# Performance work log

Measured on AMD Instinct MI355X. Metric: run time of the kernel, lower is better.

## Reference

```python
import jax, jax.numpy as jnp
import numpy as np

B, S, D = 4, 2048, 1024
H = 16
HD = D // H  # 64
MASKED_BIAS = jnp.float32(-10000.0)


def setup_inputs() -> dict:
    key = jax.random.key(0)
    ks = jax.random.split(key, 5)
    std = 0.02
    return {
        "hidden_states": jax.random.normal(ks[0], (B, S, D), jnp.float32),
        "Wq": jax.random.normal(ks[1], (D, D), jnp.float32) * std,
        "bq": jnp.zeros((D,), jnp.float32),
        "Wk": jax.random.normal(ks[2], (D, D), jnp.float32) * std,
        "bk": jnp.zeros((D,), jnp.float32),
        "Wv": jax.random.normal(ks[3], (D, D), jnp.float32) * std,
        "bv": jnp.zeros((D,), jnp.float32),
        "Wo": jax.random.normal(ks[4], (D, D), jnp.float32) * std,
        "bo": jnp.zeros((D,), jnp.float32),
    }


def _split_heads(x):
    # [B, S, D] -> [B, H, S, HD]
    return x.reshape(B, S, H, HD).transpose(0, 2, 1, 3)


def reference(hidden_states, Wq, bq, Wk, bk, Wv, bv, Wo, bo):
    q = _split_heads(hidden_states @ Wq + bq)
    k = _split_heads(hidden_states @ Wk + bk)
    v = _split_heads(hidden_states @ Wv + bv)

    # scores [B, H, S, S], scaled by sqrt(head_dim) (scale=True)
    w = jnp.einsum("bhqd,bhkd->bhqk", q, k) / jnp.sqrt(jnp.float32(HD))
    causal = jnp.tril(jnp.ones((S, S), dtype=bool))  # [S, S]
    w = jnp.where(causal[None, None], w, MASKED_BIAS)
    w = jax.nn.softmax(w, axis=-1)
    # attn_pdrop = 0.0 -> dropout is identity

    a = jnp.einsum("bhqk,bhkd->bhqd", w, v)  # [B, H, S, HD]
    a = a.transpose(0, 2, 1, 3).reshape(B, S, D)  # merge heads
    out = a @ Wo + bo
    # resid_pdrop = 0.0 -> identity
    return out
```

## Files before the change

kernel.cpp:

```cpp
#include <hip/hip_runtime.h>
#include <stdint.h>

typedef unsigned short u16;
typedef __bf16 bf16x2 __attribute__((ext_vector_type(2)));
typedef __bf16 bf16x8 __attribute__((ext_vector_type(8)));
typedef float f32x4 __attribute__((ext_vector_type(4)));
typedef float f32x16 __attribute__((ext_vector_type(16)));
typedef unsigned int u32x4 __attribute__((ext_vector_type(4)));
typedef u16 u16x8 __attribute__((ext_vector_type(8)));
typedef u16 u16x4 __attribute__((ext_vector_type(4)));

#define MFMA16(a, b, c) __builtin_amdgcn_mfma_f32_16x16x32_bf16((a), (b), (c), 0, 0, 0)
#define MFMA32(a, b, c) __builtin_amdgcn_mfma_f32_32x32x16_bf16((a), (b), (c), 0, 0, 0)

#define QSCALE 0.18033688011112042f

#if defined(__has_builtin)
#if __has_builtin(__builtin_amdgcn_exp2f)
#define EXP2(x) __builtin_amdgcn_exp2f(x)
#endif
#endif
#ifndef EXP2
#define EXP2(x) __expf((x) * 0.6931471805599453f)
#endif

__device__ __forceinline__ u16 f2bf(float f) {
  return __builtin_bit_cast(u16, (__bf16)f);
}

__device__ __forceinline__ unsigned cvtpk(float lo, float hi) {
  bf16x2 t;
  t[0] = (__bf16)lo;
  t[1] = (__bf16)hi;
  return __builtin_bit_cast(unsigned, t);
}

__device__ __forceinline__ bf16x8 load_frag(const u16* lds_base, int byteoff) {
  u32x4 v = *(const u32x4*)((const char*)lds_base + byteoff);
  return __builtin_bit_cast(bf16x8, v);
}

#define GLOAD_LDS16(gp, lp)                                                        \
  __builtin_amdgcn_global_load_lds((const __attribute__((address_space(1))) void*)(gp), \
                                   (__attribute__((address_space(3))) void*)(lp), 16, 0, 0)

template <int ROWS>
__device__ __forceinline__ void stage_tile(const u16* __restrict__ src, int ld, u16* lds,
                                           int tid) {
  constexpr int SLOTS = ROWS * 8;
#pragma unroll
  for (int it = 0; it < SLOTS / 256; ++it) {
    const int s = it * 256 + tid;
    const int row = s >> 3;
    const int seg = (s & 7) ^ (row & 7);
    const u16* g = src + row * ld + seg * 8;
    u16* l = lds + (it * 256 + (tid & ~63)) * 8;
    GLOAD_LDS16(g, l);
  }
}


__global__ __launch_bounds__(256) void cvt_x(const float* __restrict__ in,
                                             u16* __restrict__ out) {
  const int i = (int)blockIdx.x * 256 + (int)threadIdx.x;
  const float4 a = ((const float4*)in)[2 * i];
  const float4 b = ((const float4*)in)[2 * i + 1];
  u16x8 o;
  o[0] = f2bf(a.x); o[1] = f2bf(a.y); o[2] = f2bf(a.z); o[3] = f2bf(a.w);
  o[4] = f2bf(b.x); o[5] = f2bf(b.y); o[6] = f2bf(b.z); o[7] = f2bf(b.w);
  ((u16x8*)out)[i] = o;
}

__global__ __launch_bounds__(256) void cvt_w_t(const float* __restrict__ W,
                                               u16* __restrict__ Wt) {
  __shared__ u16 t[64][65];
  const int tid = (int)threadIdx.x;
  const int r = tid >> 2;
  const int cs = (tid & 3) * 16;
  const int tr = (int)blockIdx.y * 64;
  const int tc = (int)blockIdx.x * 64;
#pragma unroll
  for (int i = 0; i < 16; i += 4) {
    const float4 v = *(const float4*)&W[(size_t)(tr + r) * 1024 + tc + cs + i];
    t[r][cs + i + 0] = f2bf(v.x);
    t[r][cs + i + 1] = f2bf(v.y);
    t[r][cs + i + 2] = f2bf(v.z);
    t[r][cs + i + 3] = f2bf(v.w);
  }
  __syncthreads();
  u16 tmp[16];
#pragma unroll
  for (int i = 0; i < 16; ++i) tmp[i] = t[cs + i][r];
  u16x8 o0, o1;
#pragma unroll
  for (int i = 0; i < 8; ++i) { o0[i] = tmp[i]; o1[i] = tmp[8 + i]; }
  *(u16x8*)&Wt[(size_t)(tc + r) * 1024 + tr + cs] = o0;
  *(u16x8*)&Wt[(size_t)(tc + r) * 1024 + tr + cs + 8] = o1;
}


__device__ __forceinline__ size_t vfrag_addr(int row, int col) {
  const int b = row >> 11, s = row & 2047;
  const int h = col >> 6, d = col & 63;
  return ((size_t)((b * 16 + h) * 32 + (s >> 6))) * 4096 + (size_t)(d >> 5) * 2048 +
         (size_t)((s & 63) >> 4) * 512 + (size_t)((d & 31) | (((s >> 3) & 1) << 5)) * 8 +
         (s & 7);
}

__device__ __forceinline__ size_t kfrag_addr(int row, int col) {
  const int b = row >> 11, s = row & 2047;
  const int h = col >> 6, d = col & 63;
  return ((size_t)((b * 16 + h) * 64 + (s >> 5))) * 2048 + (size_t)(d >> 4) * 512 +
         (size_t)((s & 31) | (((d >> 3) & 1) << 5)) * 8 + (d & 7);
}


__device__ __forceinline__ void gemm_core(const u16* __restrict__ Abase,
                                          const u16* __restrict__ Bbase, u16* lds, int tid,
                                          int wm, int wn, int lr, int lg,
                                          f32x4 (&acc)[4][4]) {
  constexpr int K = 1024;
  for (int k0 = 0; k0 < K; k0 += 64) {
    stage_tile<128>(Abase + k0, K, lds, tid);
    stage_tile<128>(Bbase + k0, K, lds + 128 * 64, tid);
    __syncthreads();
#pragma unroll
    for (int ks = 0; ks < 2; ++ks) {
      bf16x8 af[4], bf[4];
#pragma unroll
      for (int i = 0; i < 4; ++i) {
        const int ar = wm * 64 + i * 16 + lr;
        af[i] = load_frag(lds, ar * 128 + ((ks * 64 + lg * 16) ^ ((ar & 7) << 4)));
        const int br = wn * 64 + i * 16 + lr;
        bf[i] = load_frag(lds + 128 * 64, br * 128 + ((ks * 64 + lg * 16) ^ ((br & 7) << 4)));
      }
#pragma unroll
      for (int mf = 0; mf < 4; ++mf)
#pragma unroll
        for (int nf = 0; nf < 4; ++nf) acc[mf][nf] = MFMA16(af[mf], bf[nf], acc[mf][nf]);
    }
    __syncthreads();
  }
}


__global__ __launch_bounds__(256) void gemm_qkv(const u16* __restrict__ A,
                                                const u16* __restrict__ Bq,
                                                const u16* __restrict__ Bk,
                                                const u16* __restrict__ Bv,
                                                const float* __restrict__ bq,
                                                const float* __restrict__ bk,
                                                const float* __restrict__ bv,
                                                u16* __restrict__ Qo, u16* __restrict__ Ko,
                                                u16* __restrict__ Vo) {
  __shared__ __align__(16) u16 lds[2 * 128 * 64];
  const int tid = (int)threadIdx.x;
  const int w = tid >> 6, lane = tid & 63;
  const int wm = w >> 1, wn = w & 1;
  const int lr = lane & 15, lg = lane >> 4;
  const int g = (int)blockIdx.x;
  const int m_idx = g >> 3, nt = g & 7;
  const int mt = (int)blockIdx.y;

  const u16* Bt = m_idx == 0 ? Bq : (m_idx == 1 ? Bk : Bv);
  const float* bias = m_idx == 0 ? bq : (m_idx == 1 ? bk : bv);

  f32x4 acc[4][4] = {};
  gemm_core(A + (size_t)mt * 128 * 1024, Bt + (size_t)nt * 128 * 1024, lds, tid, wm, wn, lr,
            lg, acc);

#pragma unroll
  for (int mf = 0; mf < 4; ++mf) {
#pragma unroll
    for (int nf = 0; nf < 4; ++nf) {
      const int col = nt * 128 + wn * 64 + nf * 16 + lr;
      const float bv2 = bias[col];
#pragma unroll
      for (int r = 0; r < 4; ++r) {
        const int row = mt * 128 + wm * 64 + mf * 16 + lg * 4 + r;
        const float v = acc[mf][nf][r] + bv2;
        if (m_idx == 0) {
          Qo[(size_t)row * 1024 + col] = f2bf(v * QSCALE);
        } else if (m_idx == 1) {
          Ko[kfrag_addr(row, col)] = f2bf(v);
        } else {
          Vo[vfrag_addr(row, col)] = f2bf(v);
        }
      }
    }
  }
}


__global__ __launch_bounds__(256) void gemm_out(const u16* __restrict__ A,
                                                const u16* __restrict__ Bt,
                                                const float* __restrict__ bias,
                                                float* __restrict__ Cout) {
  __shared__ __align__(16) u16 lds[2 * 128 * 64];
  const int tid = (int)threadIdx.x;
  const int w = tid >> 6, lane = tid & 63;
  const int wm = w >> 1, wn = w & 1;
  const int lr = lane & 15, lg = lane >> 4;
  const int mt = (int)blockIdx.y, nt = (int)blockIdx.x;

  f32x4 acc[4][4] = {};
  gemm_core(A + (size_t)mt * 128 * 1024, Bt + (size_t)nt * 128 * 1024, lds, tid, wm, wn, lr,
            lg, acc);

#pragma unroll
  for (int mf = 0; mf < 4; ++mf) {
#pragma unroll
    for (int nf = 0; nf < 4; ++nf) {
      const int col = nt * 128 + wn * 64 + nf * 16 + lr;
      const float bv = bias[col];
#pragma unroll
      for (int r = 0; r < 4; ++r) {
        const int row = mt * 128 + wm * 64 + mf * 16 + lg * 4 + r;
        Cout[(size_t)row * 1024 + col] = acc[mf][nf][r] + bv;
      }
    }
  }
}


__device__ __forceinline__ void loadK(bf16x8 (&kf)[2][4], const u16* __restrict__ p) {
#pragma unroll
  for (int sb = 0; sb < 2; ++sb)
#pragma unroll
    for (int dk = 0; dk < 4; ++dk)
      kf[sb][dk] = *(const bf16x8*)(p + sb * 2048 + dk * 512);
}

__device__ __forceinline__ void attn_tile(const bf16x8 (&kf)[2][4],
                                          const u16* __restrict__ vp_tile,
                                          const bf16x8 (&qf)[4], const int hi,
                                          const bool masked, const int tmask, f32x16& o0,
                                          f32x16& o1, float& m_run, float& l_run) {
  bf16x8 vf[2][4];
#pragma unroll
  for (int db = 0; db < 2; ++db)
#pragma unroll
    for (int ks = 0; ks < 4; ++ks)
      vf[db][ks] = *(const bf16x8*)(vp_tile + db * 2048 + ks * 512);

  f32x16 p0 = {}, p1 = {};
#pragma unroll
  for (int dk = 0; dk < 4; ++dk) {
    p0 = MFMA32(kf[0][dk], qf[dk], p0);
    p1 = MFMA32(kf[1][dk], qf[dk], p1);
  }

  if (masked) {
#pragma unroll
    for (int r = 0; r < 16; ++r) {
      const int kl = (r & 3) + 8 * (r >> 2) + 4 * hi;
      if (kl > tmask) p0[r] = -1.0e30f;
      if (kl + 32 > tmask) p1[r] = -1.0e30f;
    }
  }

  float mx = -3.0e38f;
#pragma unroll
  for (int r = 0; r < 16; ++r) mx = fmaxf(mx, fmaxf(p0[r], p1[r]));
  mx = fmaxf(mx, __shfl_xor(mx, 32));

  if (__any(mx > m_run + 11.5416f)) {
    const float mnew = fmaxf(m_run, mx);
    const float alpha = EXP2(m_run - mnew);
    m_run = mnew;
    l_run *= alpha;
#pragma unroll
    for (int r = 0; r < 16; ++r) { o0[r] *= alpha; o1[r] *= alpha; }
  }

  float rs = 0.0f;
#pragma unroll
  for (int r = 0; r < 16; ++r) {
    p0[r] = EXP2(p0[r] - m_run);
    p1[r] = EXP2(p1[r] - m_run);
    rs += p0[r] + p1[r];
  }
  rs += __shfl_xor(rs, 32);
  l_run += rs;

  unsigned c[16];
#pragma unroll
  for (int j = 0; j < 8; ++j) {
    c[j] = cvtpk(p0[2 * j], p0[2 * j + 1]);
    c[8 + j] = cvtpk(p1[2 * j], p1[2 * j + 1]);
  }
  bf16x8 pf[4];
#pragma unroll
  for (int ks = 0; ks < 4; ++ks) {
    const int base = (ks >> 1) * 8 + (ks & 1) * 4;
    auto s0 = __builtin_amdgcn_permlane32_swap(c[base + 0], c[base + 2], false, false);
    auto s1 = __builtin_amdgcn_permlane32_swap(c[base + 1], c[base + 3], false, false);
    u32x4 wv;
    wv[0] = s0[0];
    wv[1] = s1[0];
    wv[2] = s0[1];
    wv[3] = s1[1];
    pf[ks] = __builtin_bit_cast(bf16x8, wv);
  }

#pragma unroll
  for (int ks = 0; ks < 4; ++ks) {
    o0 = MFMA32(vf[0][ks], pf[ks], o0);
    o1 = MFMA32(vf[1][ks], pf[ks], o1);
  }
}

__global__ __launch_bounds__(64) void attn_fwd(const u16* __restrict__ Qb,
                                               const u16* __restrict__ Kf,
                                               const u16* __restrict__ Vf,
                                               u16* __restrict__ Ab) {
  const int lane = (int)threadIdx.x;
  const int ln = lane & 31, hi = lane >> 5;

  const int id = (int)blockIdx.x;
  const int xcd = id & 7;
  const int bh = (xcd << 3) | ((id >> 3) & 7);
  const int pair = id >> 6;
  const int b = bh >> 4, h = bh & 15;

  const u16* kp = Kf + (size_t)bh * 131072 + lane * 8;
  const u16* vp = Vf + (size_t)bh * 131072 + lane * 8;

#pragma unroll 1
  for (int pass = 0; pass < 2; ++pass) {
    const int qs = pass ? 63 - pair : pair;
    const int wq = qs * 32;
    const int qrow = wq + ln;

    const u16* qp = Qb + (size_t)(b * 2048 + qrow) * 1024 + h * 64 + hi * 8;
    bf16x8 qf[4];
#pragma unroll
    for (int dk = 0; dk < 4; ++dk) qf[dk] = *(const bf16x8*)(qp + dk * 16);

    f32x16 o0 = {}, o1 = {};
    float m_run = -3.0e38f, l_run = 0.0f;

    const int nt = (qs >> 1) + 1;
    bf16x8 kA[2][4], kB[2][4];
    loadK(kA, kp);
    int i = 0;
    while (i + 2 <= nt) {
      loadK(kB, kp + (size_t)(i + 1) * 4096);
      attn_tile(kA, vp + (size_t)i * 4096, qf, hi, false, 0, o0, o1, m_run, l_run);
      const int nx = (i + 2 < nt) ? i + 2 : i + 1;
      loadK(kA, kp + (size_t)nx * 4096);
      attn_tile(kB, vp + (size_t)(i + 1) * 4096, qf, hi, i + 2 == nt, qrow - (i + 1) * 64,
                o0, o1, m_run, l_run);
      i += 2;
    }
    if (i < nt)
      attn_tile(kA, vp + (size_t)i * 4096, qf, hi, true, qrow - i * 64, o0, o1, m_run,
                l_run);

    const float inv = 1.0f / l_run;
    u16* op = Ab + (size_t)(b * 2048 + qrow) * 1024 + h * 64;
#pragma unroll
    for (int rr = 0; rr < 4; ++rr) {
      u16x4 s0v, s1v;
#pragma unroll
      for (int cc = 0; cc < 4; ++cc) {
        s0v[cc] = f2bf(o0[rr * 4 + cc] * inv);
        s1v[cc] = f2bf(o1[rr * 4 + cc] * inv);
      }
      *(u16x4*)(op + rr * 8 + hi * 4) = s0v;
      *(u16x4*)(op + 32 + rr * 8 + hi * 4) = s1v;
    }
  }
}


extern "C" void kernel_launch(void* const* d_in, const int* in_sizes, int n_in, void* d_out,
                              int out_size, void* d_ws, size_t ws_size, hipStream_t stream) {
  const float* X = (const float*)d_in[0];
  const float* Wq = (const float*)d_in[1];
  const float* bq = (const float*)d_in[2];
  const float* Wk = (const float*)d_in[3];
  const float* bk = (const float*)d_in[4];
  const float* Wv = (const float*)d_in[5];
  const float* bv = (const float*)d_in[6];
  const float* Wo = (const float*)d_in[7];
  const float* bo = (const float*)d_in[8];
  float* out = (float*)d_out;

  u16* ws = (u16*)d_ws;
  u16* Xb = ws;
  u16* Wqt = Xb + 8388608;
  u16* Wkt = Wqt + 1048576;
  u16* Wvt = Wkt + 1048576;
  u16* Wot = Wvt + 1048576;
  u16* Qb = Wot + 1048576;
  u16* Kf = Qb + 8388608;
  u16* Vf = Kf + 8388608;
  u16* Ab = Vf + 8388608;

  cvt_x<<<4096, 256, 0, stream>>>(X, Xb);
  dim3 wtg(16, 16);
  cvt_w_t<<<wtg, 256, 0, stream>>>(Wq, Wqt);
  cvt_w_t<<<wtg, 256, 0, stream>>>(Wk, Wkt);
  cvt_w_t<<<wtg, 256, 0, stream>>>(Wv, Wvt);
  cvt_w_t<<<wtg, 256, 0, stream>>>(Wo, Wot);

  dim3 qkvg(24, 64);
  gemm_qkv<<<qkvg, 256, 0, stream>>>(Xb, Wqt, Wkt, Wvt, bq, bk, bv, Qb, Kf, Vf);

  attn_fwd<<<2048, 64, 0, stream>>>(Qb, Kf, Vf, Ab);

  dim3 gg(8, 64);
  gemm_out<<<gg, 256, 0, stream>>>(Ab, Wot, bo, out);
}
```

Baseline: 190.1 us.

## Double-buffer GEMM LDS tiles and batch weight conversions into one launch

The shared GEMM core now keeps two LDS buffers. It issues the async global-to-LDS loads for the next K tile before running the MFMAs on the current tile, so there is one barrier per step instead of two. Separately, the four weight transpose-and-convert launches are merged into one launch with a z grid dimension, cutting launch overhead. The cost is double the LDS per block (64KB), which may lower occupancy for the GEMM kernels.

```diff
diff --git a/kernel.cpp b/kernel.cpp
--- a/kernel.cpp
+++ b/kernel.cpp
@@ -71,8 +71,16 @@
   ((u16x8*)out)[i] = o;
 }
 
-__global__ __launch_bounds__(256) void cvt_w_t(const float* __restrict__ W,
-                                               u16* __restrict__ Wt) {
+__global__ __launch_bounds__(256) void cvt_w_t4(const float* __restrict__ W0,
+                                                const float* __restrict__ W1,
+                                                const float* __restrict__ W2,
+                                                const float* __restrict__ W3,
+                                                u16* __restrict__ T0, u16* __restrict__ T1,
+                                                u16* __restrict__ T2, u16* __restrict__ T3) {
+  const int z = (int)blockIdx.z;
+  const float* W = z == 0 ? W0 : (z == 1 ? W1 : (z == 2 ? W2 : W3));
+  u16* Wt = z == 0 ? T0 : (z == 1 ? T1 : (z == 2 ? T2 : T3));
+
   __shared__ u16 t[64][65];
   const int tid = (int)threadIdx.x;
   const int r = tid >> 2;
@@ -115,32 +123,44 @@
 }
 
 
+__device__ __forceinline__ void compute_tile(const u16* __restrict__ buf, int wm, int wn,
+                                             int lr, int lg, f32x4 (&acc)[4][4]) {
+#pragma unroll
+  for (int ks = 0; ks < 2; ++ks) {
+    bf16x8 af[4], bf[4];
+#pragma unroll
+    for (int i = 0; i < 4; ++i) {
+      const int ar = wm * 64 + i * 16 + lr;
+      af[i] = load_frag(buf, ar * 128 + ((ks * 64 + lg * 16) ^ ((ar & 7) << 4)));
+      const int br = wn * 64 + i * 16 + lr;
+      bf[i] = load_frag(buf + 8192, br * 128 + ((ks * 64 + lg * 16) ^ ((br & 7) << 4)));
+    }
+#pragma unroll
+    for (int mf = 0; mf < 4; ++mf)
+#pragma unroll
+      for (int nf = 0; nf < 4; ++nf) acc[mf][nf] = MFMA16(af[mf], bf[nf], acc[mf][nf]);
+  }
+}
+
 __device__ __forceinline__ void gemm_core(const u16* __restrict__ Abase,
                                           const u16* __restrict__ Bbase, u16* lds, int tid,
                                           int wm, int wn, int lr, int lg,
                                           f32x4 (&acc)[4][4]) {
   constexpr int K = 1024;
-  for (int k0 = 0; k0 < K; k0 += 64) {
-    stage_tile<128>(Abase + k0, K, lds, tid);
-    stage_tile<128>(Bbase + k0, K, lds + 128 * 64, tid);
+  stage_tile<128>(Abase, K, lds, tid);
+  stage_tile<128>(Bbase, K, lds + 8192, tid);
+  __syncthreads();
+  int cur = 0;
+#pragma unroll 1
+  for (int k0 = 64; k0 < K; k0 += 64) {
+    u16* nbuf = lds + (cur ^ 1) * 16384;
+    stage_tile<128>(Abase + k0, K, nbuf, tid);
+    stage_tile<128>(Bbase + k0, K, nbuf + 8192, tid);
+    compute_tile(lds + cur * 16384, wm, wn, lr, lg, acc);
     __syncthreads();
-#pragma unroll
-    for (int ks = 0; ks < 2; ++ks) {
-      bf16x8 af[4], bf[4];
-#pragma unroll
-      for (int i = 0; i < 4; ++i) {
-        const int ar = wm * 64 + i * 16 + lr;
-        af[i] = load_frag(lds, ar * 128 + ((ks * 64 + lg * 16) ^ ((ar & 7) << 4)));
-        const int br = wn * 64 + i * 16 + lr;
-        bf[i] = load_frag(lds + 128 * 64, br * 128 + ((ks * 64 + lg * 16) ^ ((br & 7) << 4)));
-      }
-#pragma unroll
-      for (int mf = 0; mf < 4; ++mf)
-#pragma unroll
-        for (int nf = 0; nf < 4; ++nf) acc[mf][nf] = MFMA16(af[mf], bf[nf], acc[mf][nf]);
-    }
-    __syncthreads();
-  }
+    cur ^= 1;
+  }
+  compute_tile(lds + cur * 16384, wm, wn, lr, lg, acc);
 }
 
 
@@ -153,7 +173,7 @@
                                                 const float* __restrict__ bv,
                                                 u16* __restrict__ Qo, u16* __restrict__ Ko,
                                                 u16* __restrict__ Vo) {
-  __shared__ __align__(16) u16 lds[2 * 128 * 64];
+  __shared__ __align__(16) u16 lds[32768];
   const int tid = (int)threadIdx.x;
   const int w = tid >> 6, lane = tid & 63;
   const int wm = w >> 1, wn = w & 1;
@@ -196,7 +216,7 @@
                                                 const u16* __restrict__ Bt,
                                                 const float* __restrict__ bias,
                                                 float* __restrict__ Cout) {
-  __shared__ __align__(16) u16 lds[2 * 128 * 64];
+  __shared__ __align__(16) u16 lds[32768];
   const int tid = (int)threadIdx.x;
   const int w = tid >> 6, lane = tid & 63;
   const int wm = w >> 1, wn = w & 1;
@@ -399,11 +419,8 @@
   u16* Ab = Vf + 8388608;
 
   cvt_x<<<4096, 256, 0, stream>>>(X, Xb);
-  dim3 wtg(16, 16);
-  cvt_w_t<<<wtg, 256, 0, stream>>>(Wq, Wqt);
-  cvt_w_t<<<wtg, 256, 0, stream>>>(Wk, Wkt);
-  cvt_w_t<<<wtg, 256, 0, stream>>>(Wv, Wvt);
-  cvt_w_t<<<wtg, 256, 0, stream>>>(Wo, Wot);
+  dim3 wtg(16, 16, 4);
+  cvt_w_t4<<<wtg, 256, 0, stream>>>(Wq, Wk, Wv, Wo, Wqt, Wkt, Wvt, Wot);
 
   dim3 qkvg(24, 64);
   gemm_qkv<<<qkvg, 256, 0, stream>>>(Xb, Wqt, Wkt, Wvt, bq, bk, bv, Qb, Kf, Vf);
```

Result: faster. 173.8 us (-8.6%).
